# Performance work log

Hardware: AMD Instinct MI355X
Metric: run time of the kernel (lower is better)

The kernel has to match this reference:

```python
import jax, jax.numpy as jnp
import numpy as np

S_N = 100000   # number of students (embedding rows)
K_N = 30       # knowledge dim; must equal stu_dim=30 per the torch code
N_OUT = 1024   # number of exercises / output dim
B = 4096       # batch size
K_SEL = 3      # k_n_select
NVARS = 2 ** K_SEL - 2  # 6


def setup_inputs() -> dict:
    key = jax.random.key(0)
    ks = jax.random.split(key, 12)
    stu_id = jax.random.randint(ks[0], (B,), 0, S_N)
    exer_id = jax.random.randint(ks[1], (B,), 0, N_OUT)  # unused by forward, kept for fidelity
    kn_emb = jax.random.normal(ks[2], (B, K_N), jnp.float32)  # unused by forward
    # q matrix: exactly 3 ones per row -> sorted column indices (matches boolean-mask gather order)
    rng = np.random.default_rng(0)
    q_idx = np.stack([np.sort(rng.choice(K_N, K_SEL, replace=False)) for _ in range(N_OUT)])
    q_idx = jnp.asarray(q_idx, dtype=jnp.int32)  # [N_OUT, 3]
    emb = jax.random.normal(ks[3], (S_N, 30), jnp.float32) * 0.05
    fm_vars = jnp.abs(jax.random.normal(ks[4], (NVARS, N_OUT), jnp.float32)) * 0.1 + (1.0 / K_SEL)
    def lin(k, fan_out, fan_in):
        std = (2.0 / (fan_in + fan_out)) ** 0.5  # xavier normal
        return jax.random.normal(k, (fan_out, fan_in), jnp.float32) * std
    w1 = lin(ks[5], 256, N_OUT); b1 = jnp.zeros((256,), jnp.float32)
    w2 = lin(ks[6], 128, 256);   b2 = jnp.zeros((128,), jnp.float32)
    w3 = lin(ks[7], N_OUT, 128); b3 = jnp.zeros((N_OUT,), jnp.float32)
    return {"stu_id": stu_id, "exer_id": exer_id, "kn_emb": kn_emb, "q_idx": q_idx,
            "emb": emb, "fm_vars": fm_vars,
            "w1": w1, "b1": b1, "w2": w2, "b2": b2, "w3": w3, "b3": b3}


def _chi_fm(fm_vars):
    # fuzzy-measure construction for k_n_select=3 (subset lattice hardcoded, matches torch loop)
    chi = jnp.abs(fm_vars)            # [6, N_OUT]
    f0, f1 = chi[0], chi[1]
    f2 = jnp.maximum(f0, f1) + chi[2]
    f3 = chi[3]
    f4 = jnp.maximum(f3, f0) + chi[4]
    f5 = jnp.maximum(f3, f1) + chi[5]
    FM = jnp.stack([f0, f1, f2, f3, f4, f5, jnp.ones_like(f0)], axis=0)  # [7, N_OUT]
    return jnp.minimum(FM, 1.0).T     # [N_OUT, 7]


def reference(stu_id, exer_id, kn_emb, q_idx, emb, fm_vars, w1, b1, w2, b2, w3, b3):
    stu = jnp.take(emb, stu_id, axis=0)          # [B, 30]
    sel = jax.nn.sigmoid(stu)                     # [B, K_N]
    inputs = sel[:, q_idx]                        # gather -> [B, N_OUT, 3]
    idx = jnp.argsort(-inputs, axis=2)            # descending sort indices
    sv = jnp.take_along_axis(inputs, idx, axis=2) # sorted values, descending
    # diff with trailing zero: sv[k] - sv[k+1]
    diffs = sv - jnp.concatenate([sv[:, :, 1:], jnp.zeros_like(sv[:, :, :1])], axis=2)
    out_idx = jnp.cumsum(2 ** idx, axis=2) - 1    # subset node index in [0, 6], distinct per row
    bI = jnp.arange(inputs.shape[0])[:, None, None]
    nI = jnp.arange(inputs.shape[1])[None, :, None]
    alpha = jnp.zeros(inputs.shape[:2] + (NVARS + 1,), sv.dtype).at[bI, nI, out_idx].set(diffs)
    FM = _chi_fm(fm_vars)                          # [N_OUT, 7]
    C = jnp.sum(alpha * FM[None], axis=2)          # Choquet integral [B, N_OUT]
    h = jax.nn.relu(C @ w1.T + b1)                 # dropout is identity in eval
    h = jax.nn.relu(h @ w2.T + b2)
    return jax.nn.sigmoid(h @ w3.T + b3)           # [B, N_OUT]
```

## Files before the change

### kernel.cpp

```cpp
#include <hip/hip_runtime.h>
#include <math.h>

#define K_N   30
#define N_OUT 1024
#define BB    4096

typedef unsigned short ushort_t;
typedef __attribute__((ext_vector_type(8))) short bf16x8;
typedef __attribute__((ext_vector_type(4))) float f32x4;
typedef __attribute__((ext_vector_type(4))) int int4v;
typedef __attribute__((ext_vector_type(4))) float float4v;
typedef __attribute__((ext_vector_type(4))) short short4v;

#define GLOBAL_AS(p) ((const __attribute__((address_space(1))) void*)(p))
#define LDS_AS(p)    ((__attribute__((address_space(3))) void*)(p))

__device__ __forceinline__ ushort_t f2bf(float x) {
  union { float f; unsigned u; } a; a.f = x;
  unsigned r = a.u + 0x7FFFu + ((a.u >> 16) & 1u);
  return (ushort_t)(r >> 16);
}
__device__ __forceinline__ float bf2f(ushort_t h) {
  union { float f; unsigned u; } a; a.u = ((unsigned)h) << 16;
  return a.f;
}

__global__ __launch_bounds__(256) void cicdm_choquet_split(
    const int* __restrict__ stu_id, const int* __restrict__ q_idx,
    const float* __restrict__ emb, const float* __restrict__ fm_vars,
    const float* __restrict__ w1, const float* __restrict__ w2,
    const float* __restrict__ w3, ushort_t* __restrict__ Chi,
    ushort_t* __restrict__ Clo, ushort_t* __restrict__ w1h,
    ushort_t* __restrict__ w1l, ushort_t* __restrict__ w2h,
    ushort_t* __restrict__ w2l, ushort_t* __restrict__ w3h,
    ushort_t* __restrict__ w3l) {
  __shared__ float s[K_N];
  const int b = blockIdx.x;
  const int tid = threadIdx.x;

  if (tid < 104) {
    int idx = b * 104 + tid;
    float v;
    ushort_t *ph, *pl;
    int off;
    if (idx < 262144) {
      off = idx; v = w1[off]; ph = w1h; pl = w1l;
    } else if (idx < 294912) {
      off = idx - 262144; v = w2[off]; ph = w2h; pl = w2l;
    } else {
      off = idx - 294912; v = w3[off]; ph = w3h; pl = w3l;
    }
    ushort_t h = f2bf(v);
    ph[off] = h;
    pl[off] = f2bf(v - bf2f(h));
  }

  if (tid < K_N) {
    float x = emb[(long)stu_id[b] * K_N + tid];
    s[tid] = 1.f / (1.f + expf(-x));
  }
  __syncthreads();

  const int n0 = tid * 4;
  int qs[12];
  *(int4v*)(qs + 0) = *(const int4v*)(q_idx + n0 * 3 + 0);
  *(int4v*)(qs + 4) = *(const int4v*)(q_idx + n0 * 3 + 4);
  *(int4v*)(qs + 8) = *(const int4v*)(q_idx + n0 * 3 + 8);
  float4v c0v = *(const float4v*)(fm_vars + 0 * N_OUT + n0);
  float4v c1v = *(const float4v*)(fm_vars + 1 * N_OUT + n0);
  float4v c2v = *(const float4v*)(fm_vars + 2 * N_OUT + n0);
  float4v c3v = *(const float4v*)(fm_vars + 3 * N_OUT + n0);
  float4v c4v = *(const float4v*)(fm_vars + 4 * N_OUT + n0);
  float4v c5v = *(const float4v*)(fm_vars + 5 * N_OUT + n0);

  ushort_t hv[4], lv[4];
#pragma unroll
  for (int j = 0; j < 4; ++j) {
    float v0 = s[qs[3 * j]], v1 = s[qs[3 * j + 1]], v2 = s[qs[3 * j + 2]];
    bool c01 = v1 > v0, c02 = v2 > v0, c12 = v2 > v1;
    int r0 = (int)c01 + (int)c02;
    int r1 = (int)(!c01) + (int)c12;
    int p0 = (r0 == 0) ? 0 : ((r1 == 0) ? 1 : 2);
    int p1 = (r0 == 1) ? 0 : ((r1 == 1) ? 1 : 2);
    int p2 = 3 - p0 - p1;
    float sv0 = (p0 == 0) ? v0 : ((p0 == 1) ? v1 : v2);
    float sv1 = (p1 == 0) ? v0 : ((p1 == 1) ? v1 : v2);
    float sv2 = (p2 == 0) ? v0 : ((p2 == 1) ? v1 : v2);
    float f0 = fabsf(c0v[j]), f1 = fabsf(c1v[j]);
    float f2 = fmaxf(f0, f1) + fabsf(c2v[j]);
    float f3 = fabsf(c3v[j]);
    float f4 = fmaxf(f3, f0) + fabsf(c4v[j]);
    float f5 = fmaxf(f3, f1) + fabsf(c5v[j]);
    float fm0 = (p0 == 0) ? fminf(f0, 1.f)
                          : ((p0 == 1) ? fminf(f1, 1.f) : fminf(f3, 1.f));
    float fm1 = (p2 == 2) ? fminf(f2, 1.f)
                          : ((p2 == 1) ? fminf(f4, 1.f) : fminf(f5, 1.f));
    float cval = (sv0 - sv1) * fm0 + (sv1 - sv2) * fm1 + sv2;
    ushort_t h = f2bf(cval);
    hv[j] = h;
    lv[j] = f2bf(cval - bf2f(h));
  }
  short4v H, L;
  H[0] = (short)hv[0]; H[1] = (short)hv[1]; H[2] = (short)hv[2]; H[3] = (short)hv[3];
  L[0] = (short)lv[0]; L[1] = (short)lv[1]; L[2] = (short)lv[2]; L[3] = (short)lv[3];
  *(short4v*)(Chi + (size_t)b * N_OUT + n0) = H;
  *(short4v*)(Clo + (size_t)b * N_OUT + n0) = L;
}

template <int EPI>
__global__ __launch_bounds__(256) void cicdm_gemm64(
    const ushort_t* __restrict__ Ah, const ushort_t* __restrict__ Al,
    const ushort_t* __restrict__ Wh, const ushort_t* __restrict__ Wl,
    const float* __restrict__ bias, ushort_t* __restrict__ outH,
    ushort_t* __restrict__ outL, float* __restrict__ outF, int N, int K) {
  constexpr int BM = 64, BN = 64, BK = 64, CH = 8;
  constexpr int REG = BM * BK;
  constexpr int BUF = 4 * REG;
  __shared__ __align__(16) ushort_t smem[2 * BUF];

  const int tid = threadIdx.x;
  const int lane = tid & 63;
  const int wid = tid >> 6;
  const int wr = wid >> 1, wc = wid & 1;
  const int bm = blockIdx.y * BM;
  const int bn = blockIdx.x * BN;
  const int lrow = lane & 15, lc = lane >> 4;

  auto STAGE = [&](int d, int k0) {
#pragma unroll
    for (int it = 0; it < 2; ++it) {
      int u = it * 256 + tid;
      int row = u >> 3, cp = u & 7;
      int c = cp ^ (row & 7);
      size_t ga = (size_t)(bm + row) * K + k0 + c * 8;
      size_t gw = (size_t)(bn + row) * K + k0 + c * 8;
      int lofs = (it * 256 + (wid << 6)) * 8;
      ushort_t* base = smem + d * BUF;
      __builtin_amdgcn_global_load_lds(GLOBAL_AS(Ah + ga),
                                       LDS_AS(base + lofs), 16, 0, 0);
      __builtin_amdgcn_global_load_lds(GLOBAL_AS(Al + ga),
                                       LDS_AS(base + REG + lofs), 16, 0, 0);
      __builtin_amdgcn_global_load_lds(GLOBAL_AS(Wh + gw),
                                       LDS_AS(base + 2 * REG + lofs), 16, 0, 0);
      __builtin_amdgcn_global_load_lds(GLOBAL_AS(Wl + gw),
                                       LDS_AS(base + 3 * REG + lofs), 16, 0, 0);
    }
  };

  f32x4 acc[2][2] = {};
  const int rA[2] = {wr * 32 + lrow, wr * 32 + lrow + 16};
  const int rB[2] = {wc * 32 + lrow, wc * 32 + lrow + 16};

  auto COMPUTE = [&](int d) {
    ushort_t* base = smem + d * BUF;
#pragma unroll
    for (int ks = 0; ks < 2; ++ks) {
      bf16x8 fah[2], fal[2], fbh[2], fbl[2];
#pragma unroll
      for (int i = 0; i < 2; ++i) {
        int pcA = (ks * 4 + lc) ^ (rA[i] & 7);
        int pcB = (ks * 4 + lc) ^ (rB[i] & 7);
        fah[i] = *(const bf16x8*)(base + (rA[i] * CH + pcA) * 8);
        fal[i] = *(const bf16x8*)(base + REG + (rA[i] * CH + pcA) * 8);
        fbh[i] = *(const bf16x8*)(base + 2 * REG + (rB[i] * CH + pcB) * 8);
        fbl[i] = *(const bf16x8*)(base + 3 * REG + (rB[i] * CH + pcB) * 8);
      }
#pragma unroll
      for (int mi = 0; mi < 2; ++mi)
#pragma unroll
        for (int ni = 0; ni < 2; ++ni) {
          acc[mi][ni] = __builtin_amdgcn_mfma_f32_16x16x32_bf16(
              fah[mi], fbh[ni], acc[mi][ni], 0, 0, 0);
          acc[mi][ni] = __builtin_amdgcn_mfma_f32_16x16x32_bf16(
              fah[mi], fbl[ni], acc[mi][ni], 0, 0, 0);
          acc[mi][ni] = __builtin_amdgcn_mfma_f32_16x16x32_bf16(
              fal[mi], fbh[ni], acc[mi][ni], 0, 0, 0);
        }
    }
  };

  STAGE(0, 0);
  asm volatile("s_waitcnt vmcnt(0)" ::: "memory");
  __builtin_amdgcn_s_barrier();
  const int nst = K >> 6;
  for (int t = 0; t < nst; ++t) {
    int cur = t & 1;
    if (t + 1 < nst) STAGE(cur ^ 1, (t + 1) << 6);
    COMPUTE(cur);
    asm volatile("s_waitcnt vmcnt(0)" ::: "memory");
    __builtin_amdgcn_s_barrier();
  }

#pragma unroll
  for (int mi = 0; mi < 2; ++mi) {
#pragma unroll
    for (int ni = 0; ni < 2; ++ni) {
      int col = bn + wc * 32 + ni * 16 + lrow;
      float bv = bias[col];
#pragma unroll
      for (int r = 0; r < 4; ++r) {
        int row = bm + wr * 32 + mi * 16 + lc * 4 + r;
        float v = acc[mi][ni][r] + bv;
        if (EPI == 0) {
          v = fmaxf(v, 0.f);
          ushort_t h = f2bf(v);
          outH[(size_t)row * N + col] = h;
          outL[(size_t)row * N + col] = f2bf(v - bf2f(h));
        } else {
          outF[(size_t)row * N + col] = 1.f / (1.f + expf(-v));
        }
      }
    }
  }
}

extern "C" void kernel_launch(void* const* d_in, const int* in_sizes, int n_in,
                              void* d_out, int out_size, void* d_ws,
                              size_t ws_size, hipStream_t stream) {
  const int* stu_id = (const int*)d_in[0];
  const int* q_idx = (const int*)d_in[3];
  const float* emb = (const float*)d_in[4];
  const float* fm_vars = (const float*)d_in[5];
  const float* w1 = (const float*)d_in[6];
  const float* b1 = (const float*)d_in[7];
  const float* w2 = (const float*)d_in[8];
  const float* b2 = (const float*)d_in[9];
  const float* w3 = (const float*)d_in[10];
  const float* b3 = (const float*)d_in[11];
  float* out = (float*)d_out;

  char* ws = (char*)d_ws;
  size_t off = 0;
  auto alloc = [&](size_t bytes) {
    void* p = ws + off;
    off += (bytes + 255) & ~(size_t)255;
    return p;
  };
  ushort_t* Chi = (ushort_t*)alloc((size_t)BB * N_OUT * 2);
  ushort_t* Clo = (ushort_t*)alloc((size_t)BB * N_OUT * 2);
  ushort_t* w1h = (ushort_t*)alloc(256 * N_OUT * 2);
  ushort_t* w1l = (ushort_t*)alloc(256 * N_OUT * 2);
  ushort_t* w2h = (ushort_t*)alloc(128 * 256 * 2);
  ushort_t* w2l = (ushort_t*)alloc(128 * 256 * 2);
  ushort_t* w3h = (ushort_t*)alloc(N_OUT * 128 * 2);
  ushort_t* w3l = (ushort_t*)alloc(N_OUT * 128 * 2);
  ushort_t* h1h = (ushort_t*)alloc((size_t)BB * 256 * 2);
  ushort_t* h1l = (ushort_t*)alloc((size_t)BB * 256 * 2);
  ushort_t* h2h = (ushort_t*)alloc((size_t)BB * 128 * 2);
  ushort_t* h2l = (ushort_t*)alloc((size_t)BB * 128 * 2);

  cicdm_choquet_split<<<BB, 256, 0, stream>>>(
      stu_id, q_idx, emb, fm_vars, w1, w2, w3, Chi, Clo, w1h, w1l, w2h, w2l,
      w3h, w3l);

  cicdm_gemm64<0><<<dim3(4, 64), 256, 0, stream>>>(
      Chi, Clo, w1h, w1l, b1, h1h, h1l, nullptr, 256, 1024);
  cicdm_gemm64<0><<<dim3(2, 64), 256, 0, stream>>>(
      h1h, h1l, w2h, w2l, b2, h2h, h2l, nullptr, 128, 256);
  cicdm_gemm64<1><<<dim3(16, 64), 256, 0, stream>>>(
      h2h, h2l, w3h, w3l, b3, nullptr, nullptr, out, 1024, 128);
}
```

Baseline: 128.0 us.

## Fuse Choquet and three-layer MLP into one persistent kernel per 16-row tile

Replaces the Choquet kernel plus three separate GEMM launches with one fused kernel. Each 512-thread block computes Choquet values for 16 batch rows and keeps them in LDS as split bf16 hi/lo. It then runs all three MLP layers from LDS, streaming weights through per-wave double buffers. This removes the global round trips of C, h1 and h2 and two launches, but weights are re-read by every block, and only 256 blocks with about 152KB of LDS each may limit occupancy and MFMA utilisation. Weight splitting moves to its own small kernel.

Measured after the change: 144.5 us. 12.9% more time.

```diff
diff --git a/kernel.cpp b/kernel.cpp
--- a/kernel.cpp
+++ b/kernel.cpp
@@ -4,16 +4,17 @@
 #define K_N   30
 #define N_OUT 1024
 #define BB    4096
+#define SMEM_BYTES 155648
 
 typedef unsigned short ushort_t;
 typedef __attribute__((ext_vector_type(8))) short bf16x8;
 typedef __attribute__((ext_vector_type(4))) float f32x4;
-typedef __attribute__((ext_vector_type(4))) int int4v;
-typedef __attribute__((ext_vector_type(4))) float float4v;
-typedef __attribute__((ext_vector_type(4))) short short4v;
 
 #define GLOBAL_AS(p) ((const __attribute__((address_space(1))) void*)(p))
 #define LDS_AS(p)    ((__attribute__((address_space(3))) void*)(p))
+
+#define MFMA(a, b, c) (c) = __builtin_amdgcn_mfma_f32_16x16x32_bf16((a), (b), (c), 0, 0, 0)
+#define MF3(ah, al, bh, bl, c) do { MFMA(ah, bh, c); MFMA(ah, bl, c); MFMA(al, bh, c); } while (0)
 
 __device__ __forceinline__ ushort_t f2bf(float x) {
   union { float f; unsigned u; } a; a.f = x;
@@ -25,192 +26,253 @@
   return a.f;
 }
 
-__global__ __launch_bounds__(256) void cicdm_choquet_split(
-    const int* __restrict__ stu_id, const int* __restrict__ q_idx,
-    const float* __restrict__ emb, const float* __restrict__ fm_vars,
+__device__ __forceinline__ float choquet_one(float v0, float v1, float v2,
+                                             float F0, float F1, float F2,
+                                             float F3, float F4, float F5) {
+  bool c01 = v1 > v0, c02 = v2 > v0, c12 = v2 > v1;
+  int r0 = (int)c01 + (int)c02;
+  int r1 = (int)(!c01) + (int)c12;
+  int p0 = (r0 == 0) ? 0 : ((r1 == 0) ? 1 : 2);
+  int p1 = (r0 == 1) ? 0 : ((r1 == 1) ? 1 : 2);
+  int p2 = 3 - p0 - p1;
+  float sv0 = (p0 == 0) ? v0 : ((p0 == 1) ? v1 : v2);
+  float sv1 = (p1 == 0) ? v0 : ((p1 == 1) ? v1 : v2);
+  float sv2 = (p2 == 0) ? v0 : ((p2 == 1) ? v1 : v2);
+  float fm0 = (p0 == 0) ? F0 : ((p0 == 1) ? F1 : F3);
+  float fm1 = (p2 == 2) ? F2 : ((p2 == 1) ? F4 : F5);
+  return (sv0 - sv1) * fm0 + (sv1 - sv2) * fm1 + sv2;
+}
+
+__global__ __launch_bounds__(512) void cicdm_split(
     const float* __restrict__ w1, const float* __restrict__ w2,
-    const float* __restrict__ w3, ushort_t* __restrict__ Chi,
-    ushort_t* __restrict__ Clo, ushort_t* __restrict__ w1h,
+    const float* __restrict__ w3, ushort_t* __restrict__ w1h,
     ushort_t* __restrict__ w1l, ushort_t* __restrict__ w2h,
     ushort_t* __restrict__ w2l, ushort_t* __restrict__ w3h,
     ushort_t* __restrict__ w3l) {
-  __shared__ float s[K_N];
-  const int b = blockIdx.x;
-  const int tid = threadIdx.x;
-
-  if (tid < 104) {
-    int idx = b * 104 + tid;
-    float v;
-    ushort_t *ph, *pl;
-    int off;
-    if (idx < 262144) {
-      off = idx; v = w1[off]; ph = w1h; pl = w1l;
-    } else if (idx < 294912) {
-      off = idx - 262144; v = w2[off]; ph = w2h; pl = w2l;
-    } else {
-      off = idx - 294912; v = w3[off]; ph = w3h; pl = w3l;
-    }
-    ushort_t h = f2bf(v);
-    ph[off] = h;
-    pl[off] = f2bf(v - bf2f(h));
-  }
-
-  if (tid < K_N) {
-    float x = emb[(long)stu_id[b] * K_N + tid];
-    s[tid] = 1.f / (1.f + expf(-x));
+  int i = blockIdx.x * 512 + threadIdx.x;
+  float v;
+  ushort_t *ph, *pl;
+  int off;
+  if (i < 262144) {
+    off = i; v = w1[off]; ph = w1h; pl = w1l;
+  } else if (i < 294912) {
+    off = i - 262144; v = w2[off]; ph = w2h; pl = w2l;
+  } else {
+    off = i - 294912; v = w3[off]; ph = w3h; pl = w3l;
+  }
+  ushort_t h = f2bf(v);
+  ph[off] = h;
+  pl[off] = f2bf(v - bf2f(h));
+}
+
+__global__ __launch_bounds__(512, 2) void cicdm_fused(
+    const int* __restrict__ stu_id, const int* __restrict__ q_idx,
+    const float* __restrict__ emb, const float* __restrict__ fm_vars,
+    const float* __restrict__ b1, const float* __restrict__ b2,
+    const float* __restrict__ b3, const ushort_t* __restrict__ w1h,
+    const ushort_t* __restrict__ w1l, const ushort_t* __restrict__ w2h,
+    const ushort_t* __restrict__ w2l, const ushort_t* __restrict__ w3h,
+    const ushort_t* __restrict__ w3l, float* __restrict__ out) {
+  extern __shared__ __align__(16) char dsm[];
+  ushort_t* sC = (ushort_t*)dsm;
+  ushort_t* wq = (ushort_t*)(dsm + 65536 + (threadIdx.x >> 6) * 8192);
+  float* sSel = (float*)(dsm + 65536);
+  ushort_t* sH1 = (ushort_t*)(dsm + 131072);
+  ushort_t* sH2 = (ushort_t*)(dsm + 147456);
+
+  const int bid = blockIdx.x, tid = threadIdx.x;
+  const int lane = tid & 63, wid = tid >> 6;
+  const int lrow = lane & 15, lc = lane >> 4;
+  const int row0 = bid * 16;
+
+  if (tid < 16 * K_N) {
+    int r = tid / K_N, c = tid % K_N;
+    float x = emb[(size_t)stu_id[row0 + r] * K_N + c];
+    sSel[r * 32 + c] = 1.f / (1.f + expf(-x));
   }
   __syncthreads();
-
-  const int n0 = tid * 4;
-  int qs[12];
-  *(int4v*)(qs + 0) = *(const int4v*)(q_idx + n0 * 3 + 0);
-  *(int4v*)(qs + 4) = *(const int4v*)(q_idx + n0 * 3 + 4);
-  *(int4v*)(qs + 8) = *(const int4v*)(q_idx + n0 * 3 + 8);
-  float4v c0v = *(const float4v*)(fm_vars + 0 * N_OUT + n0);
-  float4v c1v = *(const float4v*)(fm_vars + 1 * N_OUT + n0);
-  float4v c2v = *(const float4v*)(fm_vars + 2 * N_OUT + n0);
-  float4v c3v = *(const float4v*)(fm_vars + 3 * N_OUT + n0);
-  float4v c4v = *(const float4v*)(fm_vars + 4 * N_OUT + n0);
-  float4v c5v = *(const float4v*)(fm_vars + 5 * N_OUT + n0);
-
-  ushort_t hv[4], lv[4];
-#pragma unroll
-  for (int j = 0; j < 4; ++j) {
-    float v0 = s[qs[3 * j]], v1 = s[qs[3 * j + 1]], v2 = s[qs[3 * j + 2]];
-    bool c01 = v1 > v0, c02 = v2 > v0, c12 = v2 > v1;
-    int r0 = (int)c01 + (int)c02;
-    int r1 = (int)(!c01) + (int)c12;
-    int p0 = (r0 == 0) ? 0 : ((r1 == 0) ? 1 : 2);
-    int p1 = (r0 == 1) ? 0 : ((r1 == 1) ? 1 : 2);
-    int p2 = 3 - p0 - p1;
-    float sv0 = (p0 == 0) ? v0 : ((p0 == 1) ? v1 : v2);
-    float sv1 = (p1 == 0) ? v0 : ((p1 == 1) ? v1 : v2);
-    float sv2 = (p2 == 0) ? v0 : ((p2 == 1) ? v1 : v2);
-    float f0 = fabsf(c0v[j]), f1 = fabsf(c1v[j]);
-    float f2 = fmaxf(f0, f1) + fabsf(c2v[j]);
-    float f3 = fabsf(c3v[j]);
-    float f4 = fmaxf(f3, f0) + fabsf(c4v[j]);
-    float f5 = fmaxf(f3, f1) + fabsf(c5v[j]);
-    float fm0 = (p0 == 0) ? fminf(f0, 1.f)
-                          : ((p0 == 1) ? fminf(f1, 1.f) : fminf(f3, 1.f));
-    float fm1 = (p2 == 2) ? fminf(f2, 1.f)
-                          : ((p2 == 1) ? fminf(f4, 1.f) : fminf(f5, 1.f));
-    float cval = (sv0 - sv1) * fm0 + (sv1 - sv2) * fm1 + sv2;
-    ushort_t h = f2bf(cval);
-    hv[j] = h;
-    lv[j] = f2bf(cval - bf2f(h));
-  }
-  short4v H, L;
-  H[0] = (short)hv[0]; H[1] = (short)hv[1]; H[2] = (short)hv[2]; H[3] = (short)hv[3];
-  L[0] = (short)lv[0]; L[1] = (short)lv[1]; L[2] = (short)lv[2]; L[3] = (short)lv[3];
-  *(short4v*)(Chi + (size_t)b * N_OUT + n0) = H;
-  *(short4v*)(Clo + (size_t)b * N_OUT + n0) = L;
-}
-
-template <int EPI>
-__global__ __launch_bounds__(256) void cicdm_gemm64(
-    const ushort_t* __restrict__ Ah, const ushort_t* __restrict__ Al,
-    const ushort_t* __restrict__ Wh, const ushort_t* __restrict__ Wl,
-    const float* __restrict__ bias, ushort_t* __restrict__ outH,
-    ushort_t* __restrict__ outL, float* __restrict__ outF, int N, int K) {
-  constexpr int BM = 64, BN = 64, BK = 64, CH = 8;
-  constexpr int REG = BM * BK;
-  constexpr int BUF = 4 * REG;
-  __shared__ __align__(16) ushort_t smem[2 * BUF];
-
-  const int tid = threadIdx.x;
-  const int lane = tid & 63;
-  const int wid = tid >> 6;
-  const int wr = wid >> 1, wc = wid & 1;
-  const int bm = blockIdx.y * BM;
-  const int bn = blockIdx.x * BN;
-  const int lrow = lane & 15, lc = lane >> 4;
-
-  auto STAGE = [&](int d, int k0) {
-#pragma unroll
-    for (int it = 0; it < 2; ++it) {
-      int u = it * 256 + tid;
-      int row = u >> 3, cp = u & 7;
-      int c = cp ^ (row & 7);
-      size_t ga = (size_t)(bm + row) * K + k0 + c * 8;
-      size_t gw = (size_t)(bn + row) * K + k0 + c * 8;
-      int lofs = (it * 256 + (wid << 6)) * 8;
-      ushort_t* base = smem + d * BUF;
-      __builtin_amdgcn_global_load_lds(GLOBAL_AS(Ah + ga),
-                                       LDS_AS(base + lofs), 16, 0, 0);
-      __builtin_amdgcn_global_load_lds(GLOBAL_AS(Al + ga),
-                                       LDS_AS(base + REG + lofs), 16, 0, 0);
-      __builtin_amdgcn_global_load_lds(GLOBAL_AS(Wh + gw),
-                                       LDS_AS(base + 2 * REG + lofs), 16, 0, 0);
-      __builtin_amdgcn_global_load_lds(GLOBAL_AS(Wl + gw),
-                                       LDS_AS(base + 3 * REG + lofs), 16, 0, 0);
-    }
-  };
-
-  f32x4 acc[2][2] = {};
-  const int rA[2] = {wr * 32 + lrow, wr * 32 + lrow + 16};
-  const int rB[2] = {wc * 32 + lrow, wc * 32 + lrow + 16};
-
-  auto COMPUTE = [&](int d) {
-    ushort_t* base = smem + d * BUF;
-#pragma unroll
-    for (int ks = 0; ks < 2; ++ks) {
-      bf16x8 fah[2], fal[2], fbh[2], fbl[2];
-#pragma unroll
-      for (int i = 0; i < 2; ++i) {
-        int pcA = (ks * 4 + lc) ^ (rA[i] & 7);
-        int pcB = (ks * 4 + lc) ^ (rB[i] & 7);
-        fah[i] = *(const bf16x8*)(base + (rA[i] * CH + pcA) * 8);
-        fal[i] = *(const bf16x8*)(base + REG + (rA[i] * CH + pcA) * 8);
-        fbh[i] = *(const bf16x8*)(base + 2 * REG + (rB[i] * CH + pcB) * 8);
-        fbl[i] = *(const bf16x8*)(base + 3 * REG + (rB[i] * CH + pcB) * 8);
-      }
-#pragma unroll
-      for (int mi = 0; mi < 2; ++mi)
-#pragma unroll
-        for (int ni = 0; ni < 2; ++ni) {
-          acc[mi][ni] = __builtin_amdgcn_mfma_f32_16x16x32_bf16(
-              fah[mi], fbh[ni], acc[mi][ni], 0, 0, 0);
-          acc[mi][ni] = __builtin_amdgcn_mfma_f32_16x16x32_bf16(
-              fah[mi], fbl[ni], acc[mi][ni], 0, 0, 0);
-          acc[mi][ni] = __builtin_amdgcn_mfma_f32_16x16x32_bf16(
-              fal[mi], fbh[ni], acc[mi][ni], 0, 0, 0);
+  {
+    const int n0 = tid * 2;
+    const int qa0 = q_idx[n0 * 3 + 0], qa1 = q_idx[n0 * 3 + 1],
+              qa2 = q_idx[n0 * 3 + 2];
+    const int qb0 = q_idx[n0 * 3 + 3], qb1 = q_idx[n0 * 3 + 4],
+              qb2 = q_idx[n0 * 3 + 5];
+    float fa[6], fb[6];
+#pragma unroll
+    for (int v = 0; v < 6; ++v) {
+      fa[v] = fabsf(fm_vars[v * N_OUT + n0]);
+      fb[v] = fabsf(fm_vars[v * N_OUT + n0 + 1]);
+    }
+    float A0 = fminf(fa[0], 1.f), A1 = fminf(fa[1], 1.f), A3 = fminf(fa[3], 1.f);
+    float A2 = fminf(fmaxf(fa[0], fa[1]) + fa[2], 1.f);
+    float A4 = fminf(fmaxf(fa[3], fa[0]) + fa[4], 1.f);
+    float A5 = fminf(fmaxf(fa[3], fa[1]) + fa[5], 1.f);
+    float B0 = fminf(fb[0], 1.f), B1 = fminf(fb[1], 1.f), B3 = fminf(fb[3], 1.f);
+    float B2 = fminf(fmaxf(fb[0], fb[1]) + fb[2], 1.f);
+    float B4 = fminf(fmaxf(fb[3], fb[0]) + fb[4], 1.f);
+    float B5 = fminf(fmaxf(fb[3], fb[1]) + fb[5], 1.f);
+    const int kc = n0 >> 3, wi = n0 & 7;
+#pragma unroll 4
+    for (int r = 0; r < 16; ++r) {
+      const float* sr = sSel + r * 32;
+      float cA = choquet_one(sr[qa0], sr[qa1], sr[qa2], A0, A1, A2, A3, A4, A5);
+      float cB = choquet_one(sr[qb0], sr[qb1], sr[qb2], B0, B1, B2, B3, B4, B5);
+      ushort_t hA = f2bf(cA), hB = f2bf(cB);
+      ushort_t lA = f2bf(cA - bf2f(hA)), lB = f2bf(cB - bf2f(hB));
+      int byo = r * 2048 + ((kc ^ (r & 7)) * 8 + wi) * 2;
+      *(unsigned*)((char*)sC + byo) = (unsigned)hA | ((unsigned)hB << 16);
+      *(unsigned*)((char*)sC + 32768 + byo) = (unsigned)lA | ((unsigned)lB << 16);
+    }
+  }
+  __syncthreads();
+
+  {
+    auto stage = [&](int cur, int kc) {
+#pragma unroll
+      for (int j = 0; j < 2; ++j) {
+        int col = wid * 32 + j * 16 + lrow;
+        const ushort_t* s0 = w1h + (size_t)col * 1024 + kc * 32 + lc * 8;
+        const ushort_t* s1 = w1l + (size_t)col * 1024 + kc * 32 + lc * 8;
+        __builtin_amdgcn_global_load_lds(GLOBAL_AS(s0),
+            LDS_AS(wq + cur * 2048 + j * 1024), 16, 0, 0);
+        __builtin_amdgcn_global_load_lds(GLOBAL_AS(s1),
+            LDS_AS(wq + cur * 2048 + j * 1024 + 512), 16, 0, 0);
+      }
+    };
+    f32x4 acc0 = {}, acc1 = {};
+    stage(0, 0);
+#pragma unroll 2
+    for (int kc = 0; kc < 32; ++kc) {
+      int cur = kc & 1;
+      if (kc < 31) {
+        stage(cur ^ 1, kc + 1);
+        asm volatile("s_waitcnt vmcnt(4)" ::: "memory");
+      } else {
+        asm volatile("s_waitcnt vmcnt(0)" ::: "memory");
+      }
+      int pA = (kc * 4 + lc) ^ (lrow & 7);
+      bf16x8 ah = *(const bf16x8*)(sC + lrow * 1024 + pA * 8);
+      bf16x8 al = *(const bf16x8*)(sC + 16384 + lrow * 1024 + pA * 8);
+      bf16x8 b0h = *(const bf16x8*)(wq + cur * 2048 + lane * 8);
+      bf16x8 b0l = *(const bf16x8*)(wq + cur * 2048 + 512 + lane * 8);
+      bf16x8 b1h = *(const bf16x8*)(wq + cur * 2048 + 1024 + lane * 8);
+      bf16x8 b1l = *(const bf16x8*)(wq + cur * 2048 + 1536 + lane * 8);
+      MF3(ah, al, b0h, b0l, acc0);
+      MF3(ah, al, b1h, b1l, acc1);
+    }
+#pragma unroll
+    for (int j = 0; j < 2; ++j) {
+      f32x4 a = j ? acc1 : acc0;
+      int col = wid * 32 + j * 16 + lrow;
+      float bv = b1[col];
+      int kc = col >> 3, wi = col & 7;
+#pragma unroll
+      for (int rr = 0; rr < 4; ++rr) {
+        int r = lc * 4 + rr;
+        float v = fmaxf(a[rr] + bv, 0.f);
+        ushort_t h = f2bf(v);
+        int byo = r * 512 + ((kc ^ (r & 7)) * 8 + wi) * 2;
+        *(ushort_t*)((char*)sH1 + byo) = h;
+        *(ushort_t*)((char*)sH1 + 8192 + byo) = f2bf(v - bf2f(h));
+      }
+    }
+  }
+  __syncthreads();
+
+  {
+    auto stage = [&](int cur, int ks) {
+      int col = wid * 16 + lrow;
+      const ushort_t* s0 = w2h + (size_t)col * 256 + ks * 32 + lc * 8;
+      const ushort_t* s1 = w2l + (size_t)col * 256 + ks * 32 + lc * 8;
+      __builtin_amdgcn_global_load_lds(GLOBAL_AS(s0), LDS_AS(wq + cur * 2048),
+                                       16, 0, 0);
+      __builtin_amdgcn_global_load_lds(GLOBAL_AS(s1),
+                                       LDS_AS(wq + cur * 2048 + 512), 16, 0, 0);
+    };
+    f32x4 acc = {};
+    stage(0, 0);
+#pragma unroll 2
+    for (int ks = 0; ks < 8; ++ks) {
+      int cur = ks & 1;
+      if (ks < 7) {
+        stage(cur ^ 1, ks + 1);
+        asm volatile("s_waitcnt vmcnt(2)" ::: "memory");
+      } else {
+        asm volatile("s_waitcnt vmcnt(0)" ::: "memory");
+      }
+      int pA = (ks * 4 + lc) ^ (lrow & 7);
+      bf16x8 ah = *(const bf16x8*)(sH1 + lrow * 256 + pA * 8);
+      bf16x8 al = *(const bf16x8*)(sH1 + 4096 + lrow * 256 + pA * 8);
+      bf16x8 bh = *(const bf16x8*)(wq + cur * 2048 + lane * 8);
+      bf16x8 bl = *(const bf16x8*)(wq + cur * 2048 + 512 + lane * 8);
+      MF3(ah, al, bh, bl, acc);
+    }
+    int col = wid * 16 + lrow;
+    float bv = b2[col];
+    int kc = col >> 3, wi = col & 7;
+#pragma unroll
+    for (int rr = 0; rr < 4; ++rr) {
+      int r = lc * 4 + rr;
+      float v = fmaxf(acc[rr] + bv, 0.f);
+      ushort_t h = f2bf(v);
+      int byo = r * 256 + ((kc ^ (r & 7)) * 8 + wi) * 2;
+      *(ushort_t*)((char*)sH2 + byo) = h;
+      *(ushort_t*)((char*)sH2 + 4096 + byo) = f2bf(v - bf2f(h));
+    }
+  }
+  __syncthreads();
+
+  {
+    auto stage = [&](int cur, int u) {
+      int ks = u >> 2, cp = u & 3;
+#pragma unroll
+      for (int j = 0; j < 2; ++j) {
+        int col = wid * 128 + cp * 32 + j * 16 + lrow;
+        const ushort_t* s0 = w3h + (size_t)col * 128 + ks * 32 + lc * 8;
+        const ushort_t* s1 = w3l + (size_t)col * 128 + ks * 32 + lc * 8;
+        __builtin_amdgcn_global_load_lds(GLOBAL_AS(s0),
+            LDS_AS(wq + cur * 2048 + j * 1024), 16, 0, 0);
+        __builtin_amdgcn_global_load_lds(GLOBAL_AS(s1),
+            LDS_AS(wq + cur * 2048 + j * 1024 + 512), 16, 0, 0);
+      }
+    };
+    f32x4 acc[8] = {};
+    bf16x8 ah = {}, al = {};
+    stage(0, 0);
+#pragma unroll
+    for (int u = 0; u < 16; ++u) {
+      int cur = u & 1, ks = u >> 2, cp = u & 3;
+      if (u < 15) {
+        stage(cur ^ 1, u + 1);
+        asm volatile("s_waitcnt vmcnt(4)" ::: "memory");
+      } else {
+        asm volatile("s_waitcnt vmcnt(0)" ::: "memory");
+      }
+      if (cp == 0) {
+        int pA = (ks * 4 + lc) ^ (lrow & 7);
+        ah = *(const bf16x8*)(sH2 + lrow * 128 + pA * 8);
+        al = *(const bf16x8*)(sH2 + 2048 + lrow * 128 + pA * 8);
+      }
+      bf16x8 b0h = *(const bf16x8*)(wq + cur * 2048 + lane * 8);
+      bf16x8 b0l = *(const bf16x8*)(wq + cur * 2048 + 512 + lane * 8);
+      bf16x8 b1h = *(const bf16x8*)(wq + cur * 2048 + 1024 + lane * 8);
+      bf16x8 b1l = *(const bf16x8*)(wq + cur * 2048 + 1536 + lane * 8);
+      MF3(ah, al, b0h, b0l, acc[cp * 2 + 0]);
+      MF3(ah, al, b1h, b1l, acc[cp * 2 + 1]);
+    }
+#pragma unroll
+    for (int cp = 0; cp < 4; ++cp)
+#pragma unroll
+      for (int j = 0; j < 2; ++j) {
+        int col = wid * 128 + cp * 32 + j * 16 + lrow;
+        float bv = b3[col];
+#pragma unroll
+        for (int rr = 0; rr < 4; ++rr) {
+          int row = row0 + lc * 4 + rr;
+          float v = acc[cp * 2 + j][rr] + bv;
+          out[(size_t)row * N_OUT + col] = 1.f / (1.f + expf(-v));
         }
-    }
-  };
-
-  STAGE(0, 0);
-  asm volatile("s_waitcnt vmcnt(0)" ::: "memory");
-  __builtin_amdgcn_s_barrier();
-  const int nst = K >> 6;
-  for (int t = 0; t < nst; ++t) {
-    int cur = t & 1;
-    if (t + 1 < nst) STAGE(cur ^ 1, (t + 1) << 6);
-    COMPUTE(cur);
-    asm volatile("s_waitcnt vmcnt(0)" ::: "memory");
-    __builtin_amdgcn_s_barrier();
-  }
-
-#pragma unroll
-  for (int mi = 0; mi < 2; ++mi) {
-#pragma unroll
-    for (int ni = 0; ni < 2; ++ni) {
-      int col = bn + wc * 32 + ni * 16 + lrow;
-      float bv = bias[col];
-#pragma unroll
-      for (int r = 0; r < 4; ++r) {
-        int row = bm + wr * 32 + mi * 16 + lc * 4 + r;
-        float v = acc[mi][ni][r] + bv;
-        if (EPI == 0) {
-          v = fmaxf(v, 0.f);
-          ushort_t h = f2bf(v);
-          outH[(size_t)row * N + col] = h;
-          outL[(size_t)row * N + col] = f2bf(v - bf2f(h));
-        } else {
-          outF[(size_t)row * N + col] = 1.f / (1.f + expf(-v));
-        }
-      }
-    }
+      }
   }
 }
 
@@ -236,27 +298,20 @@
     off += (bytes + 255) & ~(size_t)255;
     return p;
   };
-  ushort_t* Chi = (ushort_t*)alloc((size_t)BB * N_OUT * 2);
-  ushort_t* Clo = (ushort_t*)alloc((size_t)BB * N_OUT * 2);
   ushort_t* w1h = (ushort_t*)alloc(256 * N_OUT * 2);
   ushort_t* w1l = (ushort_t*)alloc(256 * N_OUT * 2);
   ushort_t* w2h = (ushort_t*)alloc(128 * 256 * 2);
   ushort_t* w2l = (ushort_t*)alloc(128 * 256 * 2);
   ushort_t* w3h = (ushort_t*)alloc(N_OUT * 128 * 2);
   ushort_t* w3l = (ushort_t*)alloc(N_OUT * 128 * 2);
-  ushort_t* h1h = (ushort_t*)alloc((size_t)BB * 256 * 2);
-  ushort_t* h1l = (ushort_t*)alloc((size_t)BB * 256 * 2);
-  ushort_t* h2h = (ushort_t*)alloc((size_t)BB * 128 * 2);
-  ushort_t* h2l = (ushort_t*)alloc((size_t)BB * 128 * 2);
-
-  cicdm_choquet_split<<<BB, 256, 0, stream>>>(
-      stu_id, q_idx, emb, fm_vars, w1, w2, w3, Chi, Clo, w1h, w1l, w2h, w2l,
-      w3h, w3l);
-
-  cicdm_gemm64<0><<<dim3(4, 64), 256, 0, stream>>>(
-      Chi, Clo, w1h, w1l, b1, h1h, h1l, nullptr, 256, 1024);
-  cicdm_gemm64<0><<<dim3(2, 64), 256, 0, stream>>>(
-      h1h, h1l, w2h, w2l, b2, h2h, h2l, nullptr, 128, 256);
-  cicdm_gemm64<1><<<dim3(16, 64), 256, 0, stream>>>(
-      h2h, h2l, w3h, w3l, b3, nullptr, nullptr, out, 1024, 128);
-}
+
+  (void)hipFuncSetAttribute((const void*)cicdm_fused,
+                            hipFuncAttributeMaxDynamicSharedMemorySize,
+                            SMEM_BYTES);
+
+  cicdm_split<<<832, 512, 0, stream>>>(w1, w2, w3, w1h, w1l, w2h, w2l, w3h,
+                                       w3l);
+  cicdm_fused<<<256, 512, SMEM_BYTES, stream>>>(stu_id, q_idx, emb, fm_vars,
+                                                b1, b2, b3, w1h, w1l, w2h, w2l,
+                                                w3h, w3l, out);
+}
```
